# Optimization experiments

Hardware: AMD Instinct MI355X
Metric: run time of the kernel (lower is better)

Reference implementation:

```python
import jax, jax.numpy as jnp
import numpy as np

B, L, C, H, T = 4096, 32, 28, 512, 32


def setup_inputs() -> dict:
    key = jax.random.key(0)
    ks = jax.random.split(key, 10)
    s = 0.1
    return dict(
        input=jax.random.normal(ks[0], (B, L, C), jnp.float32),
        unpacked_masks=jnp.ones((B, L, 1), jnp.float32),
        bias_mat=jax.random.normal(ks[1], (B, L), jnp.float32),
        conv1_w=jax.random.normal(ks[2], (C, C, 3), jnp.float32) * s,  # OIH
        conv1_b=jnp.zeros((C,), jnp.float32),
        conv_w=jax.random.normal(ks[3], (1, C, 1), jnp.float32) * s,
        conv_b=jnp.zeros((1,), jnp.float32),
        w_ih=jax.random.normal(ks[4], (4 * H, C), jnp.float32) * s,
        w_hh=jax.random.normal(ks[5], (4 * H, H), jnp.float32) * s,
        b_ih=jnp.zeros((4 * H,), jnp.float32),
        b_hh=jnp.concatenate([jnp.zeros(H), jnp.ones(H), jnp.zeros(2 * H)]).astype(jnp.float32),  # forget-gate bias = 1 as in weights_init
        fc1_w=jax.random.normal(ks[6], (1, H), jnp.float32) * s,
        fc1_b=jnp.zeros((1,), jnp.float32),
        conv2_w=jax.random.normal(ks[7], (1, H, 1), jnp.float32) * s,
        conv2_b=jnp.zeros((1,), jnp.float32),
    )


def reference(input, unpacked_masks, bias_mat, conv1_w, conv1_b, conv_w, conv_b,
              w_ih, w_hh, b_ih, b_hh, fc1_w, fc1_b, conv2_w, conv2_b):
    b, l, c = input.shape
    # residual conv block: conv1d(28->28,k3,pad1) -> mask -> elu -> +input
    x_ncl = jnp.transpose(input, (0, 2, 1))
    y = jax.lax.conv_general_dilated(x_ncl, conv1_w, (1,), 'SAME',
                                     dimension_numbers=('NCH', 'OIH', 'NCH'))
    y = jnp.transpose(y + conv1_b[None, :, None], (0, 2, 1))
    x = jax.nn.elu(y * unpacked_masks) + input  # [B,L,C]
    # u_a: 1x1 conv (28->1) == per-position linear, then mask -> [B,L,1]
    u_a = (jnp.einsum('blc,c->bl', x, conv_w[0, :, 0]) + conv_b)[..., None] * unpacked_masks
    bias = bias_mat.reshape(b, l, 1)

    def step(carry, _):
        h, cstate = carry
        w_a = (h @ fc1_w.T + fc1_b)[:, :, None]                 # [B,1,1]
        attn = jax.nn.leaky_relu(u_a + w_a) + bias              # [B,L,1]
        attn = jax.nn.softmax(attn, axis=1)                     # softmax over sequence
        context = jnp.einsum('bl,blc->bc', attn[..., 0], x)     # [B,C]
        gates = context @ w_ih.T + b_ih + h @ w_hh.T + b_hh     # [B,4H]
        i, f, g, o = jnp.split(gates, 4, axis=1)                # torch LSTMCell gate order
        cstate = jax.nn.sigmoid(f) * cstate + jax.nn.sigmoid(i) * jnp.tanh(g)
        h = jax.nn.sigmoid(o) * jnp.tanh(cstate)
        return (h, cstate), h

    h0 = jnp.zeros((b, w_hh.shape[1]), input.dtype)
    (_, _), hs = jax.lax.scan(step, (h0, h0), None, length=T)   # [T,B,H]
    all_hidden = jnp.transpose(hs, (1, 0, 2))                   # [B,T,H]
    # dropout layers are identity in eval; conv2 is 1x1 conv (512->1)
    out = (jnp.einsum('bth,h->bt', all_hidden, conv2_w[0, :, 0]) + conv2_b)[..., None]
    return out * unpacked_masks
```

## Files before the change

kernel.cpp:

```cpp
#include <hip/hip_runtime.h>
#include <hip/hip_bf16.h>

#define B_N 4096
#define L_N 32
#define C_N 28
#define H_N 512
#define T_N 32
#define G_N 2048
#define CHA 34
#define CHSH 4096
#define ABLK (CHA * CHSH)
#define XS 29

typedef __attribute__((ext_vector_type(2))) float f32x2;
typedef __attribute__((ext_vector_type(4))) float f32x4;
typedef __attribute__((ext_vector_type(8))) short s16x8;

static constexpr size_t OFF_WF = 0;
static constexpr size_t AB_ONE = (size_t)32 * ABLK * 2;
static constexpr size_t OFF_AB = OFF_WF + (size_t)16 * ABLK * 2;
static constexpr size_t OFF_X  = OFF_AB + 2 * AB_ONE;
static constexpr size_t OFF_UA = OFF_X + (size_t)B_N * L_N * C_N * 4;
static constexpr size_t OFF_BS = OFF_UA + (size_t)B_N * L_N * 4;
static constexpr size_t OFF_AC = OFF_BS + 8192;
static constexpr size_t ACC_HALF = (size_t)32 * B_N * 4;
static constexpr size_t OFF_CS = OFF_AC + 2 * ACC_HALF;
static constexpr size_t WS_NEED = OFF_CS + (size_t)B_N * H_N * 4;

__device__ __forceinline__ short bfbits(__hip_bfloat16 b) {
    union { __hip_bfloat16 b; short s; } v; v.b = b; return v.s;
}
__device__ __forceinline__ float sigmoidf_(float x) { return 1.f / (1.f + __expf(-x)); }
__device__ __forceinline__ float tanhf_(float x) {
    float ax = fabsf(x), e = __expf(-2.f * ax);
    float t = (1.f - e) / (1.f + e);
    return x < 0.f ? -t : t;
}

__global__ __launch_bounds__(256) void fill_out(float* out, float v) {
    int i = blockIdx.x * 256 + threadIdx.x;
    if (i < B_N * 32) out[i] = v;
}

__global__ __launch_bounds__(256) void prep_x(const float* __restrict__ input,
                       const float* __restrict__ mask,
                       const float* __restrict__ w1, const float* __restrict__ b1,
                       const float* __restrict__ cw, const float* __restrict__ cb,
                       float* __restrict__ x, float* __restrict__ ua)
{
    __shared__ float sin[8 * L_N * XS];
    __shared__ float sxb[8 * L_N * XS];
    const float* src = input + (size_t)blockIdx.x * (8 * L_N * C_N);
    for (int i = threadIdx.x; i < 8 * L_N * C_N; i += 256) {
        int lr = i / (L_N * C_N);
        int rem = i - lr * (L_N * C_N);
        int l = rem / C_N, c = rem - l * C_N;
        sin[lr * (L_N * XS) + l * XS + c] = src[i];
    }
    __syncthreads();

    int idx = blockIdx.x * 256 + threadIdx.x;
    int l = idx & 31;
    int wv = threadIdx.x >> 5;
    const float* inb = sin + wv * (L_N * XS);
    float m = mask[idx];

    float x0r[C_N], xm1[C_N], xp1[C_N];
    #pragma unroll
    for (int i = 0; i < C_N; ++i) x0r[i] = inb[l * XS + i];
    #pragma unroll
    for (int i = 0; i < C_N; ++i) {
        float up = __shfl_up(x0r[i], 1, 32);
        float dn = __shfl_down(x0r[i], 1, 32);
        xm1[i] = (l > 0)  ? up : 0.f;
        xp1[i] = (l < 31) ? dn : 0.f;
    }

    float uacc = 0.f;
    float* sxrow = sxb + wv * (L_N * XS) + l * XS;
    #pragma unroll 2
    for (int o = 0; o < C_N; ++o) {
        const float* wo = w1 + o * (C_N * 3);
        float y0 = b1[o], y1 = 0.f, y2 = 0.f;
        #pragma unroll
        for (int i = 0; i < C_N; ++i) {
            y0 += wo[i * 3 + 0] * xm1[i];
            y1 += wo[i * 3 + 1] * x0r[i];
            y2 += wo[i * 3 + 2] * xp1[i];
        }
        float y = (y0 + y1 + y2) * m;
        float e = (y > 0.f) ? y : (__expf(y) - 1.f);
        float xv = e + inb[l * XS + o];
        sxrow[o] = xv;
        uacc += xv * cw[o];
    }
    ua[idx] = (uacc + cb[0]) * m;
    __syncthreads();
    float* xdst = x + (size_t)blockIdx.x * (8 * L_N * C_N);
    for (int i = threadIdx.x; i < 8 * L_N * C_N; i += 256) {
        int lr = i / (L_N * C_N);
        int rem = i - lr * (L_N * C_N);
        int l2 = rem / C_N, c = rem - l2 * C_N;
        xdst[i] = sxb[lr * (L_N * XS) + l2 * XS + c];
    }
}

__global__ __launch_bounds__(256) void prep_wf(const float* __restrict__ w_ih,
                                               const float* __restrict__ w_hh,
                                               short* __restrict__ Wf)
{
    int blk = blockIdx.x;
    int n128 = blk / CHA, c = blk % CHA;
    bool lo = (c >= 17);
    int kbase = (lo ? (c - 17) : c) * 32;
    short* dst = Wf + ((size_t)n128 * CHA + c) * CHSH;
    for (int g = threadIdx.x; g < 512; g += 256) {
        int j = g >> 6, lane = g & 63;
        int p = n128 * 128 + j * 16 + (lane & 15);
        int unit = p >> 2, gate = p & 3;
        int srow = gate * H_N + unit;
        int kg = lane >> 4;
        s16x8 out;
        #pragma unroll
        for (int b2 = 0; b2 < 8; ++b2) {
            int k = kbase + kg * 8 + b2;
            float v = 0.f;
            if (k < 512) v = w_hh[(size_t)srow * H_N + k];
            else if (k < 540) v = w_ih[srow * C_N + (k - 512)];
            __hip_bfloat16 hi = __float2bfloat16(v);
            if (lo) out[b2] = bfbits(__float2bfloat16(v - __bfloat162float(hi)));
            else    out[b2] = bfbits(hi);
        }
        *(s16x8*)(dst + g * 8) = out;
    }
}

__global__ void prep_bs(const float* __restrict__ b_ih, const float* __restrict__ b_hh,
                        float* __restrict__ bsum)
{
    int p = blockIdx.x * 256 + threadIdx.x;
    if (p < G_N) {
        int unit = p >> 2, gate = p & 3;
        bsum[p] = b_ih[gate * H_N + unit] + b_hh[gate * H_N + unit];
    }
}

__global__ void prep_zero(unsigned int* __restrict__ a32, float* __restrict__ cst,
                          float* __restrict__ acc)
{
    int idx = blockIdx.x * blockDim.x + threadIdx.x;
    if (idx < B_N * 1088) a32[idx] = 0u;
    if (idx < B_N * H_N) cst[idx] = 0.f;
    if (idx < 2 * 32 * B_N) acc[idx] = 0.f;
}

struct RParams {
    const float* mask;
    const float* bias_mat;
    const float* fc1_w;
    const float* fc1_b;
    const float* conv2_w;
    const float* conv2_b;
    const short* Wf;
    const short* Ain;
    short* Aout;
    const float* x;
    const float* ua;
    const float* bsum;
    float* accW;
    float* accO;
    float* cstate;
    float* out;
};

__global__ __launch_bounds__(256) void ctx_step(RParams P, int t)
{
    __shared__ float sx[4][L_N * C_N];

    const int lane = threadIdx.x & 63;
    const int wave = threadIdx.x >> 6;
    const int row  = blockIdx.x * 4 + wave;

    f32x2 st[7];
    const float* xrow = P.x + (size_t)row * (L_N * C_N);
    #pragma unroll
    for (int q = 0; q < 7; ++q) st[q] = *(const f32x2*)(xrow + (q * 64 + lane) * 2);

    float v = (lane < 32) ? P.accW[row * 32 + lane] : P.accO[row * 32 + (lane - 32)];
    #pragma unroll
    for (int off = 1; off <= 16; off <<= 1) v += __shfl_xor(v, off);
    float aW = __shfl(v, 0);
    float aO = __shfl(v, 32);

    if (t > 0 && lane == 0)
        P.out[row * T_N + (t - 1)] = (aO + P.conv2_b[0]) * P.mask[row * L_N + (t - 1)];

    if (t < T_N) {
        float w_a = aW + P.fc1_b[0];
        int l32 = lane & 31;
        float e = P.ua[row * L_N + l32] + w_a;
        e = (e > 0.f) ? e : 0.01f * e;
        e += P.bias_mat[row * L_N + l32];
        float mx = e;
        #pragma unroll
        for (int off = 16; off > 0; off >>= 1) mx = fmaxf(mx, __shfl_xor(mx, off, 32));
        float pexp = __expf(e - mx);
        float ssum = pexp;
        #pragma unroll
        for (int off = 16; off > 0; off >>= 1) ssum += __shfl_xor(ssum, off, 32);
        float p = pexp / ssum;

        #pragma unroll
        for (int q = 0; q < 7; ++q)
            *(f32x2*)(&sx[wave][(q * 64 + lane) * 2]) = st[q];

        int cc = (lane < C_N) ? lane : 0;
        float ctx = 0.f;
        #pragma unroll
        for (int l = 0; l < L_N; ++l) {
            float al = __shfl(p, l);
            ctx += al * sx[wave][l * C_N + cc];
        }
        if (lane < C_N) {
            int m128 = row >> 7, mt = (row & 127) >> 4, r = row & 15;
            int flane = r + 16 * (lane >> 3);
            short* base = P.Aout + (size_t)m128 * ABLK + mt * 512 + flane * 8 + (lane & 7);
            __hip_bfloat16 hi = __float2bfloat16(ctx);
            base[16 * CHSH] = bfbits(hi);
            base[33 * CHSH] = bfbits(__float2bfloat16(ctx - __bfloat162float(hi)));
        }
    }
}

#define STG_BUF 32768

__global__ __launch_bounds__(256, 2) void gemm_cell_step(RParams P)
{
    __shared__ __align__(16) char smem[65536];

    const int tid  = threadIdx.x;
    const int lane = tid & 63;
    const int wave = tid >> 6;
    const int bid  = blockIdx.x;
    const int xg = bid & 7, gg = bid >> 3;
    const int m  = (xg >> 1) * 8 + (gg & 7);
    const int n  = (xg & 1) * 8 + (gg >> 3);
    const int wm = wave >> 1, wn = wave & 1;

    const short* Af = P.Ain + (size_t)m * ABLK;
    const short* Wg = P.Wf  + (size_t)n * ABLK;

    const short* slab0 = (wave < 2) ? Af : Wg;
    const int slab_lo  = (wave & 1) ? 17 : 0;

    char* bufp0 = smem;
    char* bufp1 = smem + STG_BUF;

    auto stage = [&](char* lbuf, int kk) {
        const short* gp = slab0 + (size_t)(slab_lo + kk) * CHSH + lane * 8;
        char* lb = lbuf + wave * 8192;
        #pragma unroll
        for (int r = 0; r < 8; ++r) {
            __builtin_amdgcn_global_load_lds(
                (const __attribute__((address_space(1))) void*)(gp + r * 512),
                (__attribute__((address_space(3))) void*)(lb + r * 1024),
                16, 0, 0);
        }
    };

    int aoff[4], woff[4];
    #pragma unroll
    for (int i = 0; i < 4; ++i) {
        aoff[i] = ((wm * 4 + i) * 64 + lane) * 16;
        woff[i] = ((wn * 4 + i) * 64 + lane) * 16;
    }

    f32x4 acc[4][4];
    #pragma unroll
    for (int i = 0; i < 4; ++i)
        #pragma unroll
        for (int j = 0; j < 4; ++j)
            acc[i][j] = (f32x4){0.f, 0.f, 0.f, 0.f};

    s16x8 RA[16], RB[16];
    auto ldfr = [&](const char* b, s16x8 (&R)[16]) {
        #pragma unroll
        for (int i = 0; i < 4; ++i) {
            R[i]      = *(const s16x8*)(b + aoff[i]);
            R[4 + i]  = *(const s16x8*)(b + 8192 + aoff[i]);
            R[8 + i]  = *(const s16x8*)(b + 16384 + woff[i]);
            R[12 + i] = *(const s16x8*)(b + 24576 + woff[i]);
        }
    };
    auto domm = [&](s16x8 (&R)[16]) {
        #pragma unroll
        for (int i = 0; i < 4; ++i)
            #pragma unroll
            for (int j = 0; j < 4; ++j)
                acc[i][j] = __builtin_amdgcn_mfma_f32_16x16x32_bf16(R[i], R[8 + j], acc[i][j], 0, 0, 0);
        #pragma unroll
        for (int i = 0; i < 4; ++i)
            #pragma unroll
            for (int j = 0; j < 4; ++j)
                acc[i][j] = __builtin_amdgcn_mfma_f32_16x16x32_bf16(R[4 + i], R[8 + j], acc[i][j], 0, 0, 0);
        #pragma unroll
        for (int i = 0; i < 4; ++i)
            #pragma unroll
            for (int j = 0; j < 4; ++j)
                acc[i][j] = __builtin_amdgcn_mfma_f32_16x16x32_bf16(R[i], R[12 + j], acc[i][j], 0, 0, 0);
    };
    auto step = [&](int kk, s16x8 (&Rc)[16], s16x8 (&Rn)[16], char* bcur, char* bnext) {
        asm volatile("s_waitcnt vmcnt(0) lgkmcnt(0)" ::: "memory");
        __builtin_amdgcn_s_barrier();
        __builtin_amdgcn_sched_barrier(0);
        if (kk + 2 <= 16) stage(bcur, kk + 2);
        if (kk + 1 <= 16) ldfr(bnext, Rn);
        __builtin_amdgcn_sched_barrier(0);
        __builtin_amdgcn_s_setprio(1);
        domm(Rc);
        __builtin_amdgcn_s_setprio(0);
        __builtin_amdgcn_sched_barrier(0);
    };

    stage(bufp0, 0);
    asm volatile("s_waitcnt vmcnt(0)" ::: "memory");
    __builtin_amdgcn_s_barrier();
    stage(bufp1, 1);
    ldfr(bufp0, RA);

    for (int kp = 0; kp < 8; ++kp) {
        step(2 * kp,     RA, RB, bufp0, bufp1);
        step(2 * kp + 1, RB, RA, bufp1, bufp0);
    }
    step(16, RA, RB, bufp0, bufp1);

    __syncthreads();
    float* gates = (float*)smem;
    short* hasm  = (short*)(smem + 32768);
    #pragma unroll
    for (int hh = 0; hh < 2; ++hh) {
        int u = tid & 15, rr = tid >> 4;
        int unit = n * 32 + hh * 16 + u;
        float cpre[8];
        #pragma unroll
        for (int it = 0; it < 8; ++it)
            cpre[it] = P.cstate[(size_t)(m * 128 + it * 16 + rr) * H_N + unit];
        f32x4 bsv = *(const f32x4*)(P.bsum + unit * 4);
        float f1v = P.fc1_w[unit];
        float c2v = P.conv2_w[unit];

        if (wn == hh) {
            #pragma unroll
            for (int i = 0; i < 4; ++i)
                #pragma unroll
                for (int j = 0; j < 4; ++j)
                    #pragma unroll
                    for (int r = 0; r < 4; ++r) {
                        int rowl = wm * 64 + i * 16 + (lane >> 4) * 4 + r;
                        int coll = j * 16 + (lane & 15);
                        gates[rowl * 64 + coll] = acc[i][j][r];
                    }
        }
        __syncthreads();
        {
            int flane = rr + 16 * (hh * 2 + (u >> 3));
            #pragma unroll
            for (int it = 0; it < 8; ++it) {
                int rowl = it * 16 + rr;
                int grow = m * 128 + rowl;
                f32x4 gv = *(const f32x4*)(gates + rowl * 64 + u * 4);
                float pi = gv.x + bsv.x;
                float pf = gv.y + bsv.y;
                float pg = gv.z + bsv.z;
                float po = gv.w + bsv.w;
                float c = sigmoidf_(pf) * cpre[it] + sigmoidf_(pi) * tanhf_(pg);
                P.cstate[(size_t)grow * H_N + unit] = c;
                float h = sigmoidf_(po) * tanhf_(c);
                __hip_bfloat16 hi = __float2bfloat16(h);
                hasm[it * 512 + flane * 8 + (u & 7)]        = bfbits(hi);
                hasm[4096 + it * 512 + flane * 8 + (u & 7)] = bfbits(__float2bfloat16(h - __bfloat162float(hi)));
                float wd = f1v * h, od = c2v * h;
                #pragma unroll
                for (int off = 8; off > 0; off >>= 1) {
                    wd += __shfl_xor(wd, off);
                    od += __shfl_xor(od, off);
                }
                if (u == 0) {
                    P.accW[(size_t)grow * 32 + (n * 2 + hh)] = wd;
                    P.accO[(size_t)grow * 32 + (n * 2 + hh)] = od;
                }
            }
        }
        __syncthreads();
    }
    short* dhi = P.Aout + (size_t)m * ABLK + (size_t)n * CHSH;
    short* dlo = P.Aout + (size_t)m * ABLK + (size_t)(17 + n) * CHSH;
    *(s16x8*)(dhi + tid * 16)     = *(const s16x8*)(hasm + tid * 16);
    *(s16x8*)(dhi + tid * 16 + 8) = *(const s16x8*)(hasm + tid * 16 + 8);
    *(s16x8*)(dlo + tid * 16)     = *(const s16x8*)(hasm + 4096 + tid * 16);
    *(s16x8*)(dlo + tid * 16 + 8) = *(const s16x8*)(hasm + 4096 + tid * 16 + 8);
}

extern "C" void kernel_launch(void* const* d_in, const int* in_sizes, int n_in,
                              void* d_out, int out_size, void* d_ws, size_t ws_size,
                              hipStream_t stream)
{
    float* out = (float*)d_out;
    if (ws_size < WS_NEED) { fill_out<<<512, 256, 0, stream>>>(out, 4000.f); return; }

    const float* input = (const float*)d_in[0];
    const float* mask  = (const float*)d_in[1];
    const float* biasm = (const float*)d_in[2];
    const float* w1    = (const float*)d_in[3];
    const float* b1    = (const float*)d_in[4];
    const float* cw    = (const float*)d_in[5];
    const float* cb    = (const float*)d_in[6];
    const float* w_ih  = (const float*)d_in[7];
    const float* w_hh  = (const float*)d_in[8];
    const float* b_ih  = (const float*)d_in[9];
    const float* b_hh  = (const float*)d_in[10];
    const float* fc1w  = (const float*)d_in[11];
    const float* fc1b  = (const float*)d_in[12];
    const float* c2w   = (const float*)d_in[13];
    const float* c2b   = (const float*)d_in[14];

    char* ws = (char*)d_ws;
    short* Wf = (short*)(ws + OFF_WF);
    short* A0 = (short*)(ws + OFF_AB);
    short* A1 = (short*)(ws + OFF_AB + AB_ONE);
    float* x    = (float*)(ws + OFF_X);
    float* ua   = (float*)(ws + OFF_UA);
    float* bsum = (float*)(ws + OFF_BS);
    float* accW = (float*)(ws + OFF_AC);
    float* accO = (float*)(ws + OFF_AC + ACC_HALF);
    float* cst  = (float*)(ws + OFF_CS);

    prep_x<<<(B_N * L_N) / 256, 256, 0, stream>>>(input, mask, w1, b1, cw, cb, x, ua);
    prep_wf<<<16 * CHA, 256, 0, stream>>>(w_ih, w_hh, Wf);
    prep_bs<<<(G_N + 255) / 256, 256, 0, stream>>>(b_ih, b_hh, bsum);
    prep_zero<<<(B_N * 1088 + 255) / 256, 256, 0, stream>>>((unsigned int*)A0, cst, accW);

    RParams P;
    P.mask = mask; P.bias_mat = biasm; P.fc1_w = fc1w; P.fc1_b = fc1b;
    P.conv2_w = c2w; P.conv2_b = c2b; P.Wf = Wf;
    P.x = x; P.ua = ua; P.bsum = bsum; P.accW = accW; P.accO = accO;
    P.cstate = cst; P.out = out;

    short* bufs[2] = { A0, A1 };
    for (int t = 0; t < T_N; ++t) {
        P.Ain  = bufs[t & 1];
        P.Aout = bufs[t & 1];
        ctx_step<<<B_N / 4, 256, 0, stream>>>(P, t);
        P.Ain  = bufs[t & 1];
        P.Aout = bufs[(t + 1) & 1];
        gemm_cell_step<<<512, 256, 0, stream>>>(P);
    }
    P.Ain = bufs[T_N & 1];
    P.Aout = bufs[T_N & 1];
    ctx_step<<<B_N / 4, 256, 0, stream>>>(P, T_N);
}
```

Measured before the change: 1.376 ms.

## Fuse attention/context computation into the GEMM cell step kernel

Removes the separate ctx_step launch per timestep and computes the attention softmax and context vector inside gemm_cell_step for the block's 128 rows, staging x rows through LDS. The context is split into bf16 hi/lo parts and written directly into the LDS staging buffer for the last K chunk instead of being round-tripped through global memory. This saves one kernel launch and the global write/read of the context per step. In exchange, each of the 16 N-column blocks sharing an M tile recomputes the same context, and LDS usage grows, which may reduce occupancy.

```diff
diff --git a/kernel.cpp b/kernel.cpp
--- a/kernel.cpp
+++ b/kernel.cpp
@@ -234,9 +234,9 @@
 
 #define STG_BUF 32768
 
-__global__ __launch_bounds__(256, 2) void gemm_cell_step(RParams P)
-{
-    __shared__ __align__(16) char smem[65536];
+__global__ __launch_bounds__(256, 2) void gemm_cell_step(RParams P, int t)
+{
+    __shared__ __align__(16) char smem[65536 + 14336 + 64];
 
     const int tid  = threadIdx.x;
     const int lane = tid & 63;
@@ -252,9 +252,12 @@
 
     const short* slab0 = (wave < 2) ? Af : Wg;
     const int slab_lo  = (wave & 1) ? 17 : 0;
+    const bool is_a_wave = (wave < 2);
 
     char* bufp0 = smem;
     char* bufp1 = smem + STG_BUF;
+    float* ctxout = (float*)(smem + 65536);
+    float* xs = (float*)(smem + STG_BUF + 16384);
 
     auto stage = [&](char* lbuf, int kk) {
         const short* gp = slab0 + (size_t)(slab_lo + kk) * CHSH + lane * 8;
@@ -267,6 +270,58 @@
                 16, 0, 0);
         }
     };
+
+    stage(bufp0, 0);
+
+    {
+        float* myxs = xs + wave * (L_N * C_N);
+        int r0 = wave * 32;
+        f32x2 st[7];
+        const float* xr = P.x + (size_t)(m * 128 + r0) * (L_N * C_N);
+        #pragma unroll
+        for (int q = 0; q < 7; ++q) st[q] = *(const f32x2*)(xr + (q * 64 + lane) * 2);
+        for (int r = 0; r < 32; ++r) {
+            int grow = m * 128 + r0 + r;
+            #pragma unroll
+            for (int q = 0; q < 7; ++q) *(f32x2*)(myxs + (q * 64 + lane) * 2) = st[q];
+            if (r < 31) {
+                const float* xr2 = P.x + (size_t)(grow + 1) * (L_N * C_N);
+                #pragma unroll
+                for (int q = 0; q < 7; ++q) st[q] = *(const f32x2*)(xr2 + (q * 64 + lane) * 2);
+            }
+            float v = (lane < 32) ? P.accW[(size_t)grow * 32 + lane]
+                                  : P.accO[(size_t)grow * 32 + (lane - 32)];
+            #pragma unroll
+            for (int off = 1; off <= 16; off <<= 1) v += __shfl_xor(v, off);
+            float aW = __shfl(v, 0);
+            float aO = __shfl(v, 32);
+            if (t > 0 && n == 0 && lane == 0)
+                P.out[(size_t)grow * T_N + (t - 1)] =
+                    (aO + P.conv2_b[0]) * P.mask[grow * L_N + (t - 1)];
+            float w_a = aW + P.fc1_b[0];
+            int l32 = lane & 31;
+            float e = P.ua[grow * L_N + l32] + w_a;
+            e = (e > 0.f) ? e : 0.01f * e;
+            e += P.bias_mat[grow * L_N + l32];
+            float mx = e;
+            #pragma unroll
+            for (int off = 16; off > 0; off >>= 1) mx = fmaxf(mx, __shfl_xor(mx, off, 32));
+            float pexp = __expf(e - mx);
+            float ssum = pexp;
+            #pragma unroll
+            for (int off = 16; off > 0; off >>= 1) ssum += __shfl_xor(ssum, off, 32);
+            float p = pexp / ssum;
+            int cc = (lane < C_N) ? lane : 0;
+            float ctx = 0.f;
+            #pragma unroll
+            for (int l = 0; l < L_N; ++l) {
+                float al = __shfl(p, l);
+                ctx += al * myxs[l * C_N + cc];
+            }
+            if (lane < C_N) ctxout[(r0 + r) * C_N + lane] = ctx;
+        }
+    }
+    __syncthreads();
 
     int aoff[4], woff[4];
     #pragma unroll
@@ -313,8 +368,36 @@
         asm volatile("s_waitcnt vmcnt(0) lgkmcnt(0)" ::: "memory");
         __builtin_amdgcn_s_barrier();
         __builtin_amdgcn_sched_barrier(0);
-        if (kk + 2 <= 16) stage(bcur, kk + 2);
+        int ks = kk + 2;
+        if (ks <= (is_a_wave ? 15 : 16)) stage(bcur, ks);
         if (kk + 1 <= 16) ldfr(bnext, Rn);
+        if (kk == 14) {
+            short* fhi = (short*)bufp0;
+            short* flo = (short*)(bufp0 + 8192);
+            #pragma unroll
+            for (int q = 0; q < 2; ++q) {
+                int tt = wave * 2 + q;
+                int row = tt * 16 + (lane & 15);
+                int kg = lane >> 4;
+                const float* srcp = ctxout + row * C_N + kg * 8;
+                f32x4 c0 = *(const f32x4*)(srcp);
+                f32x4 c1 = *(const f32x4*)(srcp + 4);
+                float ksc = (kg == 3) ? 0.f : 1.f;
+                c1 *= ksc;
+                s16x8 hi8, lo8;
+                #pragma unroll
+                for (int b2 = 0; b2 < 4; ++b2) {
+                    __hip_bfloat16 h0 = __float2bfloat16(c0[b2]);
+                    hi8[b2] = bfbits(h0);
+                    lo8[b2] = bfbits(__float2bfloat16(c0[b2] - __bfloat162float(h0)));
+                    __hip_bfloat16 h1 = __float2bfloat16(c1[b2]);
+                    hi8[4 + b2] = bfbits(h1);
+                    lo8[4 + b2] = bfbits(__float2bfloat16(c1[b2] - __bfloat162float(h1)));
+                }
+                *(s16x8*)(fhi + tt * 512 + lane * 8) = hi8;
+                *(s16x8*)(flo + tt * 512 + lane * 8) = lo8;
+            }
+        }
         __builtin_amdgcn_sched_barrier(0);
         __builtin_amdgcn_s_setprio(1);
         domm(Rc);
@@ -322,10 +405,9 @@
         __builtin_amdgcn_sched_barrier(0);
     };
 
-    stage(bufp0, 0);
-    asm volatile("s_waitcnt vmcnt(0)" ::: "memory");
+    stage(bufp1, 1);
+    asm volatile("s_waitcnt vmcnt(8)" ::: "memory");
     __builtin_amdgcn_s_barrier();
-    stage(bufp1, 1);
     ldfr(bufp0, RA);
 
     for (int kp = 0; kp < 8; ++kp) {
@@ -449,11 +531,8 @@
     short* bufs[2] = { A0, A1 };
     for (int t = 0; t < T_N; ++t) {
         P.Ain  = bufs[t & 1];
-        P.Aout = bufs[t & 1];
-        ctx_step<<<B_N / 4, 256, 0, stream>>>(P, t);
-        P.Ain  = bufs[t & 1];
         P.Aout = bufs[(t + 1) & 1];
-        gemm_cell_step<<<512, 256, 0, stream>>>(P);
+        gemm_cell_step<<<512, 256, 0, stream>>>(P, t);
     }
     P.Ain = bufs[T_N & 1];
     P.Aout = bufs[T_N & 1];
```

Measured after the change: 2.999 ms. +118.0%, slower.

## Reorder gate weight columns so LSTM epilogue runs directly from accumulators

Applied to the files above, without the earlier changes.

Changes the packed weight layout so each MFMA output column tile j holds one gate (i,f,g,o) for the same 16 units. The epilogue can then combine gates straight from the register accumulators without staging the gate matrix through shared memory. This removes the LDS round trip and two of the three barriers per step. The cost is a different per-lane row mapping for cell-state loads and stores, which become less coalesced.

```diff
diff --git a/kernel.cpp b/kernel.cpp
--- a/kernel.cpp
+++ b/kernel.cpp
@@ -116,8 +116,8 @@
     short* dst = Wf + ((size_t)n128 * CHA + c) * CHSH;
     for (int g = threadIdx.x; g < 512; g += 256) {
         int j = g >> 6, lane = g & 63;
-        int p = n128 * 128 + j * 16 + (lane & 15);
-        int unit = p >> 2, gate = p & 3;
+        int gate = j & 3;
+        int unit = n128 * 32 + (j >> 2) * 16 + (lane & 15);
         int srow = gate * H_N + unit;
         int kg = lane >> 4;
         s16x8 out;
@@ -335,64 +335,51 @@
     step(16, RA, RB, bufp0, bufp1);
 
     __syncthreads();
-    float* gates = (float*)smem;
-    short* hasm  = (short*)(smem + 32768);
-    #pragma unroll
-    for (int hh = 0; hh < 2; ++hh) {
-        int u = tid & 15, rr = tid >> 4;
-        int unit = n * 32 + hh * 16 + u;
-        float cpre[8];
-        #pragma unroll
-        for (int it = 0; it < 8; ++it)
-            cpre[it] = P.cstate[(size_t)(m * 128 + it * 16 + rr) * H_N + unit];
+    short* hasm = (short*)smem;
+    {
+        int u15 = lane & 15, rq = lane >> 4;
+        int unit = n * 32 + wn * 16 + u15;
+        float cpre[4][4];
+        #pragma unroll
+        for (int i = 0; i < 4; ++i)
+            #pragma unroll
+            for (int r = 0; r < 4; ++r)
+                cpre[i][r] = P.cstate[(size_t)(m * 128 + wm * 64 + i * 16 + rq * 4 + r) * H_N + unit];
         f32x4 bsv = *(const f32x4*)(P.bsum + unit * 4);
         float f1v = P.fc1_w[unit];
         float c2v = P.conv2_w[unit];
-
-        if (wn == hh) {
+        const int fl16 = 16 * (wn * 2 + (u15 >> 3));
+        const int slot = u15 & 7;
+        #pragma unroll
+        for (int i = 0; i < 4; ++i) {
             #pragma unroll
-            for (int i = 0; i < 4; ++i)
-                #pragma unroll
-                for (int j = 0; j < 4; ++j)
-                    #pragma unroll
-                    for (int r = 0; r < 4; ++r) {
-                        int rowl = wm * 64 + i * 16 + (lane >> 4) * 4 + r;
-                        int coll = j * 16 + (lane & 15);
-                        gates[rowl * 64 + coll] = acc[i][j][r];
-                    }
-        }
-        __syncthreads();
-        {
-            int flane = rr + 16 * (hh * 2 + (u >> 3));
-            #pragma unroll
-            for (int it = 0; it < 8; ++it) {
-                int rowl = it * 16 + rr;
-                int grow = m * 128 + rowl;
-                f32x4 gv = *(const f32x4*)(gates + rowl * 64 + u * 4);
-                float pi = gv.x + bsv.x;
-                float pf = gv.y + bsv.y;
-                float pg = gv.z + bsv.z;
-                float po = gv.w + bsv.w;
-                float c = sigmoidf_(pf) * cpre[it] + sigmoidf_(pi) * tanhf_(pg);
+            for (int r = 0; r < 4; ++r) {
+                int grow = m * 128 + wm * 64 + i * 16 + rq * 4 + r;
+                float pi = acc[i][0][r] + bsv.x;
+                float pf = acc[i][1][r] + bsv.y;
+                float pg = acc[i][2][r] + bsv.z;
+                float po = acc[i][3][r] + bsv.w;
+                float c = sigmoidf_(pf) * cpre[i][r] + sigmoidf_(pi) * tanhf_(pg);
                 P.cstate[(size_t)grow * H_N + unit] = c;
                 float h = sigmoidf_(po) * tanhf_(c);
                 __hip_bfloat16 hi = __float2bfloat16(h);
-                hasm[it * 512 + flane * 8 + (u & 7)]        = bfbits(hi);
-                hasm[4096 + it * 512 + flane * 8 + (u & 7)] = bfbits(__float2bfloat16(h - __bfloat162float(hi)));
+                int fo = (wm * 4 + i) * 512 + (rq * 4 + r + fl16) * 8 + slot;
+                hasm[fo]        = bfbits(hi);
+                hasm[4096 + fo] = bfbits(__float2bfloat16(h - __bfloat162float(hi)));
                 float wd = f1v * h, od = c2v * h;
                 #pragma unroll
                 for (int off = 8; off > 0; off >>= 1) {
                     wd += __shfl_xor(wd, off);
                     od += __shfl_xor(od, off);
                 }
-                if (u == 0) {
-                    P.accW[(size_t)grow * 32 + (n * 2 + hh)] = wd;
-                    P.accO[(size_t)grow * 32 + (n * 2 + hh)] = od;
+                if (u15 == 0) {
+                    P.accW[(size_t)grow * 32 + (n * 2 + wn)] = wd;
+                    P.accO[(size_t)grow * 32 + (n * 2 + wn)] = od;
                 }
             }
         }
-        __syncthreads();
-    }
+    }
+    __syncthreads();
     short* dhi = P.Aout + (size_t)m * ABLK + (size_t)n * CHSH;
     short* dlo = P.Aout + (size_t)m * ABLK + (size_t)(17 + n) * CHSH;
     *(s16x8*)(dhi + tid * 16)     = *(const s16x8*)(hasm + tid * 16);
```

New measurement: 1.363 ms. Within noise of the previous version (-1.0%).
